# Kernel tuning notes

Hardware: AMD Instinct MI355X
Metric: run time of the kernel (lower is better)

Reference implementation:

```python
import jax, jax.numpy as jnp
import numpy as np

# Production-scale config (CIFAR-like images, PixelRNN Diagonal BiLSTM)
B, C, H, W = 32, 3, 32, 32
HC = 128   # hidden_channels
NC = 256   # num_classes


def _diag_indices(height, width):
    """Static index maps for anti-diagonal traversal of the skewed grid.

    skewed grid is (H, SW) with SW = W + H - 1. Diagonal d contains cells
    (row, col=d-row) for valid rows, processed in increasing-row order.
    Returns SW, row[D,S], col[D,S] (clipped), mask[D,S], rev[D,S] where
    rev[d, t] = len(d)-1-t maps forward step index <-> reversed step index.
    """
    SW = width + height - 1
    D = height + SW - 1
    d = np.arange(D)[:, None]
    s = np.arange(height)[None, :]
    r0 = np.maximum(0, d - (SW - 1))
    length = np.minimum(height - 1, d) - r0 + 1
    row = r0 + s
    col = d - row
    mask = s < length
    rev = np.clip(length - 1 - s, 0, height - 1)
    return SW, np.clip(row, 0, height - 1), np.clip(col, 0, SW - 1), mask, rev


def _lstm_scan(inp, mask, Wi, Wh, b):
    """Masked LSTM over all diagonals in parallel.

    inp: (B, D, S, in_dim) step-major per-diagonal inputs; mask: (D, S) bool.
    States are zero-initialized per diagonal (matching the torch module which
    resets states for every diagonal). Returns hidden outputs (B, D, S, hc).
    """
    Bb, Dd, S, _ = inp.shape
    hc = Wh.shape[1]

    def step(carry, xs):
        h, c = carry
        x_s, m = xs                       # (B, D, in_dim), (D,)
        gates = x_s @ Wi.T + b + h @ Wh.T  # (B, D, 4*hc)
        i, f, o, g = jnp.split(gates, 4, axis=-1)
        c_new = jax.nn.sigmoid(f) * c + jax.nn.sigmoid(i) * jnp.tanh(g)
        h_new = jax.nn.sigmoid(o) * jnp.tanh(c_new)
        m3 = m[None, :, None]
        return (jnp.where(m3, h_new, h), jnp.where(m3, c_new, c)), jnp.where(m3, h_new, 0.0)

    h0 = jnp.zeros((Bb, Dd, hc), inp.dtype)
    _, ys = jax.lax.scan(step, (h0, h0), (inp.transpose(2, 0, 1, 3), mask.T))
    return ys.transpose(1, 2, 0, 3)


def _forward(x, in_proj_w, in_proj_b, fwd_Wi, fwd_Wh, fwd_b,
             bwd_Wi, bwd_Wh, bwd_b, out_w, out_b):
    Bb, Cc, Hh, Ww = x.shape
    hc = in_proj_w.shape[0]
    nc = out_w.shape[0] // Cc
    SW, row, col, mask_np, rev_np = _diag_indices(Hh, Ww)
    rows = np.arange(Hh)
    cols_unskew = rows[:, None] + np.arange(Ww)[None, :]  # (H, W)

    # 1x1 input projection on normalized pixels
    xp = jnp.einsum('bchw,oc->bohw', x / 255.0, in_proj_w) + in_proj_b[None, :, None, None]

    # skew: row i shifted right by i
    skewed = jnp.zeros((Bb, hc, Hh, SW), xp.dtype).at[
        :, :, rows[:, None], cols_unskew].set(xp)

    mask = jnp.asarray(mask_np)
    # gather per-diagonal sequences: (B, D, S, hc)
    diag = jnp.where(mask[None, :, :, None],
                     skewed[:, :, row, col].transpose(0, 2, 3, 1), 0.0)

    # forward direction along each diagonal
    h_fwd = _lstm_scan(diag, mask, fwd_Wi, fwd_Wh, fwd_b)

    # backward direction: reverse steps within each diagonal, scan, un-reverse
    rev_idx = jnp.asarray(rev_np)[None, :, :, None]
    h_bwd_rev = _lstm_scan(jnp.take_along_axis(diag, rev_idx, axis=2),
                           mask, bwd_Wi, bwd_Wh, bwd_b)
    h_bwd = jnp.where(mask[None, :, :, None],
                      jnp.take_along_axis(h_bwd_rev, rev_idx, axis=2), 0.0)

    def to_grid(h):  # scatter (B, D, S, hc) back onto the skewed grid
        return jnp.zeros((Bb, hc, Hh, SW), h.dtype).at[
            :, :, row, col].add(h.transpose(0, 3, 1, 2))

    comb = jnp.concatenate([to_grid(h_fwd), to_grid(h_bwd)], axis=1)  # (B, 2hc, H, SW)

    # unskew: row i takes cols i:i+W
    un = comb[:, :, rows[:, None], cols_unskew]  # (B, 2hc, H, W)

    logits = jnp.einsum('bchw,oc->bohw', un, out_w) + out_b[None, :, None, None]
    return logits.reshape(Bb, Cc, nc, Hh, Ww)


def setup_inputs() -> dict:
    key = jax.random.key(0)
    ks = jax.random.split(key, 11)
    sc = 0.05
    return {
        'x': jax.random.uniform(ks[0], (B, C, H, W), jnp.float32) * 255.0,
        'in_proj_w': jax.random.normal(ks[1], (HC, C), jnp.float32) * sc,
        'in_proj_b': jax.random.normal(ks[2], (HC,), jnp.float32) * sc,
        'fwd_Wi': jax.random.normal(ks[3], (4 * HC, HC), jnp.float32) * sc,
        'fwd_Wh': jax.random.normal(ks[4], (4 * HC, HC), jnp.float32) * sc,
        'fwd_b': jax.random.normal(ks[5], (4 * HC,), jnp.float32) * sc,
        'bwd_Wi': jax.random.normal(ks[6], (4 * HC, HC), jnp.float32) * sc,
        'bwd_Wh': jax.random.normal(ks[7], (4 * HC, HC), jnp.float32) * sc,
        'bwd_b': jax.random.normal(ks[8], (4 * HC,), jnp.float32) * sc,
        'out_w': jax.random.normal(ks[9], (C * NC, 2 * HC), jnp.float32) * sc,
        'out_b': jax.random.normal(ks[10], (C * NC,), jnp.float32) * sc,
    }


def reference(x, in_proj_w, in_proj_b, fwd_Wi, fwd_Wh, fwd_b,
              bwd_Wi, bwd_Wh, bwd_b, out_w, out_b):
    return _forward(x, in_proj_w, in_proj_b, fwd_Wi, fwd_Wh, fwd_b,
                    bwd_Wi, bwd_Wh, bwd_b, out_w, out_b)
```

## Files before the change

kernel.cpp:

```cpp
#include <hip/hip_runtime.h>

#define Hh 32
#define Ww 32
#define SW 63
#define DD 94

typedef __attribute__((ext_vector_type(8))) short  s8v;
typedef __attribute__((ext_vector_type(4))) float  f32x4;


__device__ __forceinline__ float sigmoid_f(float v) {
    return 1.0f / (1.0f + __expf(-v));
}
__device__ __forceinline__ float tanh_f(float v) {
    float e = __expf(2.0f * v);
    return 1.0f - 2.0f / (e + 1.0f);
}
__device__ __forceinline__ unsigned short f2bf(float f) {
    unsigned int u = __builtin_bit_cast(unsigned int, f);
    unsigned int r = (u + 0x7fffu + ((u >> 16) & 1u)) >> 16;
    return (unsigned short)r;
}

__global__ void prep_wf(const float* __restrict__ fwi, const float* __restrict__ fwh,
                        const float* __restrict__ bwi, const float* __restrict__ bwh,
                        unsigned short* __restrict__ wif, unsigned short* __restrict__ whf) {
    int m = blockIdx.y;
    const float* src = (m == 0) ? fwi : (m == 1) ? fwh : (m == 2) ? bwi : bwh;
    unsigned short* dst = (m & 1) ? whf : wif;
    int dir = m >> 1;

    int t = blockIdx.x * 256 + threadIdx.x;
    int lane = t & 63;
    int kt   = (t >> 6) & 3;
    int nt   = (t >> 8) & 3;
    int wv   = (t >> 10) & 7;

    int gp = wv * 64 + nt * 16 + (lane & 15);
    int ch = gp >> 2, ty = gp & 3;
    int kbase = kt * 32 + (lane >> 4) * 8;
    const float* srow = src + (ty * 128 + ch) * 128 + kbase;

    s8v v;
    #pragma unroll
    for (int j = 0; j < 8; j++) v[j] = (short)f2bf(srow[j]);
    int off = dir * 65536 + ((wv * 4 + nt) * 4 + kt) * 512 + lane * 8;
    *reinterpret_cast<s8v*>(dst + off) = v;
}

__global__ void prep_b(const float* __restrict__ fwd_b, const float* __restrict__ bwd_b,
                       float* __restrict__ biasp) {
    int tid = threadIdx.x;
    int dir = tid >> 9;
    int gp  = tid & 511;
    int ch  = gp >> 2;
    int ty  = gp & 3;
    const float* src = dir ? bwd_b : fwd_b;
    biasp[dir * 512 + gp] = src[ty * 128 + ch];
}

__global__ void prep_ow(const float* __restrict__ ow, unsigned short* __restrict__ owb) {
    int i = blockIdx.x * 1024 + threadIdx.x;
    owb[i] = f2bf(ow[i]);
}

__global__ __launch_bounds__(512, 2) void lstm_mfma(
    const float* __restrict__ x,
    const float* __restrict__ ipw,
    const float* __restrict__ ipb,
    const unsigned short* __restrict__ whf,
    const unsigned short* __restrict__ wif,
    const float* __restrict__ biasp,
    unsigned short* __restrict__ comb)
{
    __shared__ unsigned short h_lds[2][32 * 128];
    __shared__ unsigned short xp_lds[2][32 * 128];
    __shared__ float ipw_s[384];
    __shared__ float ipb_s[128];

    const int tid  = threadIdx.x;
    const int wv   = tid >> 6;
    const int lane = tid & 63;
    const int g16  = lane >> 4;
    const int cl   = lane & 15;
    const int swz  = (cl & 7) << 3;

    const int d   = blockIdx.x >> 1;
    const int dir = blockIdx.x & 1;
    const int r0   = max(0, d - (SW - 1));
    const int rend = min(Hh - 1, d);
    const int len  = rend - r0 + 1;
    const float inv255 = 1.0f / 255.0f;

    s8v whB[4][4], wiB[4][4];
    {
        const unsigned short* whd = whf + dir * 65536;
        const unsigned short* wid = wif + dir * 65536;
        #pragma unroll
        for (int nt = 0; nt < 4; nt++)
            #pragma unroll
            for (int kt = 0; kt < 4; kt++) {
                int off = ((wv * 4 + nt) * 4 + kt) * 512 + lane * 8;
                whB[nt][kt] = *reinterpret_cast<const s8v*>(whd + off);
                wiB[nt][kt] = *reinterpret_cast<const s8v*>(wid + off);
            }
    }
    f32x4 bias4[4];
    #pragma unroll
    for (int nt = 0; nt < 4; nt++)
        bias4[nt] = *reinterpret_cast<const f32x4*>(biasp + dir * 512 + wv * 64 + nt * 16 + g16 * 4);

    if (tid < 384) ipw_s[tid] = ipw[tid];
    else if (tid < 512) ipb_s[tid - 384] = ipb[tid - 384];

    {
        unsigned int* hz = reinterpret_cast<unsigned int*>(&h_lds[0][0]);
        #pragma unroll
        for (int j = 0; j < 4; j++) hz[tid * 4 + j] = 0u;
    }
    __syncthreads();

    {
        int s0 = dir ? (len - 1) : 0;
        int row0 = r0 + s0;
        int w0 = d - 2 * row0;
        bool valid0 = ((unsigned)w0 < 32u);
        #pragma unroll
        for (int mt = 0; mt < 2; mt++) {
            int seq = mt * 16 + cl;
            float xv0 = 0, xv1 = 0, xv2 = 0;
            if (valid0) {
                const float* xb = x + seq * 3072 + row0 * 32 + w0;
                xv0 = xb[0]; xv1 = xb[1024]; xv2 = xb[2048];
            }
            #pragma unroll
            for (int nt = 0; nt < 4; nt++) {
                int ch = wv * 16 + nt * 4 + g16;
                float xpf = 0.0f;
                if (valid0)
                    xpf = ipb_s[ch] + inv255 * (xv0 * ipw_s[ch * 3] + xv1 * ipw_s[ch * 3 + 1] + xv2 * ipw_s[ch * 3 + 2]);
                xp_lds[0][(seq * 128 + ch) ^ swz] = f2bf(xpf);
            }
        }
    }
    __syncthreads();

    float cst[2][4];
    #pragma unroll
    for (int mt = 0; mt < 2; mt++)
        #pragma unroll
        for (int nt = 0; nt < 4; nt++) cst[mt][nt] = 0.0f;

    int cur = 0;
    for (int t = 0; t < len; t++) {
        int s   = dir ? (len - 1 - t) : t;
        int row = r0 + s;
        int w   = d - 2 * row;
        bool valid = ((unsigned)w < 32u);

        int s2 = dir ? (len - 2 - t) : (t + 1);
        bool have2 = (t + 1 < len);
        int row2 = r0 + s2;
        int w2 = d - 2 * row2;
        bool valid2 = have2 && ((unsigned)w2 < 32u);

        f32x4 acc[2][4];
        #pragma unroll
        for (int mt = 0; mt < 2; mt++)
            #pragma unroll
            for (int nt = 0; nt < 4; nt++) acc[mt][nt] = bias4[nt];

        #pragma unroll
        for (int kt = 0; kt < 4; kt++) {
            s8v hfr[2], xfr[2];
            #pragma unroll
            for (int mt = 0; mt < 2; mt++) {
                int idx = ((mt * 16 + cl) * 128 + kt * 32 + g16 * 8) ^ swz;
                hfr[mt] = *reinterpret_cast<const s8v*>(&h_lds[cur][idx]);
                xfr[mt] = *reinterpret_cast<const s8v*>(&xp_lds[cur][idx]);
            }
            #pragma unroll
            for (int mt = 0; mt < 2; mt++)
                #pragma unroll
                for (int nt = 0; nt < 4; nt++) {
                    acc[mt][nt] = __builtin_amdgcn_mfma_f32_16x16x32_bf16(whB[nt][kt], hfr[mt], acc[mt][nt], 0, 0, 0);
                    acc[mt][nt] = __builtin_amdgcn_mfma_f32_16x16x32_bf16(wiB[nt][kt], xfr[mt], acc[mt][nt], 0, 0, 0);
                }
        }

        int nxt = cur ^ 1;
        #pragma unroll
        for (int mt = 0; mt < 2; mt++) {
            int seq = mt * 16 + cl;
            float xv0 = 0, xv1 = 0, xv2 = 0;
            if (valid2) {
                const float* xb = x + seq * 3072 + row2 * 32 + w2;
                xv0 = xb[0]; xv1 = xb[1024]; xv2 = xb[2048];
            }
            #pragma unroll
            for (int nt = 0; nt < 4; nt++) {
                int ch = wv * 16 + nt * 4 + g16;
                float gi = acc[mt][nt][0];
                float gf = acc[mt][nt][1];
                float go = acc[mt][nt][2];
                float gg = acc[mt][nt][3];
                float c = sigmoid_f(gf) * cst[mt][nt] + sigmoid_f(gi) * tanh_f(gg);
                cst[mt][nt] = c;
                float hn = sigmoid_f(go) * tanh_f(c);
                unsigned short hq = f2bf(hn);

                int idx = (seq * 128 + ch) ^ swz;
                h_lds[nxt][idx] = hq;
                if (valid)
                    comb[((seq * 32 + row) * 32 + w) * 256 + dir * 128 + ch] = hq;
                if (have2) {
                    float xpf = 0.0f;
                    if (valid2)
                        xpf = ipb_s[ch] + inv255 * (xv0 * ipw_s[ch * 3] + xv1 * ipw_s[ch * 3 + 1] + xv2 * ipw_s[ch * 3 + 2]);
                    xp_lds[nxt][idx] = f2bf(xpf);
                }
            }
        }
        __syncthreads();
        cur = nxt;
    }
}

__global__ __launch_bounds__(256) void outproj_mfma(
    const unsigned short* __restrict__ comb,
    const unsigned short* __restrict__ owb,
    const float* __restrict__ ob,
    float* __restrict__ out)
{
    const int tid  = threadIdx.x;
    const int wave = tid >> 6;
    const int wo   = wave >> 1;
    const int wc   = wave & 1;
    const int lane = tid & 63;
    const int g16  = lane >> 4;
    const int cl   = lane & 15;

    const int o_base = blockIdx.y * 128 + wo * 64;
    const int c_base = blockIdx.x * 128 + wc * 64;

    f32x4 acc[4][4];
    #pragma unroll
    for (int of = 0; of < 4; of++)
        #pragma unroll
        for (int cf = 0; cf < 4; cf++) {
            f32x4 z = {0.f, 0.f, 0.f, 0.f};
            acc[of][cf] = z;
        }

    for (int kt = 0; kt < 8; kt++) {
        int kb = kt * 32 + g16 * 8;
        s8v a[4], b[4];
        #pragma unroll
        for (int of = 0; of < 4; of++)
            a[of] = *reinterpret_cast<const s8v*>(owb + (o_base + of * 16 + cl) * 256 + kb);
        #pragma unroll
        for (int cf = 0; cf < 4; cf++)
            b[cf] = *reinterpret_cast<const s8v*>(comb + (c_base + cf * 16 + cl) * 256 + kb);
        #pragma unroll
        for (int of = 0; of < 4; of++)
            #pragma unroll
            for (int cf = 0; cf < 4; cf++)
                acc[of][cf] = __builtin_amdgcn_mfma_f32_16x16x32_bf16(a[of], b[cf], acc[of][cf], 0, 0, 0);
    }

    #pragma unroll
    for (int of = 0; of < 4; of++) {
        f32x4 obv = *reinterpret_cast<const f32x4*>(ob + o_base + of * 16 + g16 * 4);
        #pragma unroll
        for (int cf = 0; cf < 4; cf++) {
            int cell = c_base + cf * 16 + cl;
            int bi = cell >> 10;
            int rw = cell & 1023;
            #pragma unroll
            for (int r = 0; r < 4; r++) {
                int o = o_base + of * 16 + g16 * 4 + r;
                out[(bi * 768 + o) * 1024 + rw] = acc[of][cf][r] + obv[r];
            }
        }
    }
}

extern "C" void kernel_launch(void* const* d_in, const int* in_sizes, int n_in,
                              void* d_out, int out_size, void* d_ws, size_t ws_size,
                              hipStream_t stream) {
    const float* x      = (const float*)d_in[0];
    const float* ipw    = (const float*)d_in[1];
    const float* ipb    = (const float*)d_in[2];
    const float* fwd_Wi = (const float*)d_in[3];
    const float* fwd_Wh = (const float*)d_in[4];
    const float* fwd_b  = (const float*)d_in[5];
    const float* bwd_Wi = (const float*)d_in[6];
    const float* bwd_Wh = (const float*)d_in[7];
    const float* bwd_b  = (const float*)d_in[8];
    const float* out_w  = (const float*)d_in[9];
    const float* out_b  = (const float*)d_in[10];

    char* ws = (char*)d_ws;
    unsigned short* whf   = (unsigned short*)(ws);
    unsigned short* wif   = (unsigned short*)(ws + (256 << 10));
    float*          biasp = (float*)(ws + (512 << 10));
    unsigned short* owb   = (unsigned short*)(ws + (768 << 10));
    unsigned short* comb  = (unsigned short*)(ws + (2 << 20));
    float*          out   = (float*)d_out;

    hipLaunchKernelGGL(prep_wf, dim3(64, 4), dim3(256), 0, stream,
                       fwd_Wi, fwd_Wh, bwd_Wi, bwd_Wh, wif, whf);
    hipLaunchKernelGGL(prep_b, dim3(1), dim3(1024), 0, stream,
                       fwd_b, bwd_b, biasp);
    hipLaunchKernelGGL(prep_ow, dim3(192), dim3(1024), 0, stream,
                       out_w, owb);

    hipLaunchKernelGGL(lstm_mfma, dim3(DD * 2), dim3(512), 0, stream,
                       x, ipw, ipb, whf, wif, biasp, comb);

    hipLaunchKernelGGL(outproj_mfma, dim3(256, 6), dim3(256), 0, stream,
                       comb, owb, out_b, out);
}
```

Measured before the change: 320.6 us.

## Fold input projection into Wi, precompute padding-cell LSTM states, split batch across blocks

Folds the 3-channel input projection into the LSTM input weights so the input gate contribution becomes a rank-3 affine per step, which removes the Wi MFMAs and the xp LDS buffer. Padding cells, whose input is zero, are handled by a precomputed table of h/c states after j leading padding steps, so each diagonal block runs only its valid rows. The batch is split into two 16-sequence blocks and each wave now covers 8 gate tiles, which raises the grid size. The output projection epilogue is staged through LDS so global stores are coalesced. This adds a serial single-block prep kernel and keeps the input path in fp32, so rounding differs slightly from the old bf16 path.

```diff
diff --git a/kernel.cpp b/kernel.cpp
--- a/kernel.cpp
+++ b/kernel.cpp
@@ -1,7 +1,5 @@
 #include <hip/hip_runtime.h>
 
-#define Hh 32
-#define Ww 32
 #define SW 63
 #define DD 94
 
@@ -22,41 +20,87 @@
     return (unsigned short)r;
 }
 
-__global__ void prep_wf(const float* __restrict__ fwi, const float* __restrict__ fwh,
-                        const float* __restrict__ bwi, const float* __restrict__ bwh,
-                        unsigned short* __restrict__ wif, unsigned short* __restrict__ whf) {
-    int m = blockIdx.y;
-    const float* src = (m == 0) ? fwi : (m == 1) ? fwh : (m == 2) ? bwi : bwh;
-    unsigned short* dst = (m & 1) ? whf : wif;
-    int dir = m >> 1;
-
+__global__ void prep_whf(const float* __restrict__ fwh, const float* __restrict__ bwh,
+                         unsigned short* __restrict__ whf) {
+    int dir = blockIdx.y;
+    const float* src = dir ? bwh : fwh;
     int t = blockIdx.x * 256 + threadIdx.x;
     int lane = t & 63;
     int kt   = (t >> 6) & 3;
-    int nt   = (t >> 8) & 3;
-    int wv   = (t >> 10) & 7;
-
-    int gp = wv * 64 + nt * 16 + (lane & 15);
-    int ch = gp >> 2, ty = gp & 3;
-    int kbase = kt * 32 + (lane >> 4) * 8;
-    const float* srow = src + (ty * 128 + ch) * 128 + kbase;
-
+    int nt   = (t >> 8) & 7;
+    int wv   = (t >> 11) & 3;
+    int gp  = wv * 128 + nt * 16 + (lane & 15);
+    int row = (gp & 3) * 128 + (gp >> 2);
+    int kb  = kt * 32 + (lane >> 4) * 8;
+    const float* sr = src + row * 128 + kb;
     s8v v;
     #pragma unroll
-    for (int j = 0; j < 8; j++) v[j] = (short)f2bf(srow[j]);
-    int off = dir * 65536 + ((wv * 4 + nt) * 4 + kt) * 512 + lane * 8;
-    *reinterpret_cast<s8v*>(dst + off) = v;
-}
-
-__global__ void prep_b(const float* __restrict__ fwd_b, const float* __restrict__ bwd_b,
-                       float* __restrict__ biasp) {
+    for (int j = 0; j < 8; j++) v[j] = (short)f2bf(sr[j]);
+    *reinterpret_cast<s8v*>(whf + dir * 65536 + ((wv * 8 + nt) * 4 + kt) * 512 + lane * 8) = v;
+}
+
+__global__ void prep_m1(const float* __restrict__ fwi, const float* __restrict__ bwi,
+                        const float* __restrict__ fb,  const float* __restrict__ bb,
+                        const float* __restrict__ ipw, const float* __restrict__ ipb,
+                        float* __restrict__ m1g) {
+    int t = blockIdx.x * 256 + threadIdx.x;
+    int dir = t >> 9;
+    int gp  = t & 511;
+    const float* Wi = dir ? bwi : fwi;
+    const float* bs = dir ? bb  : fb;
+    int row = (gp & 3) * 128 + (gp >> 2);
+    const float* wr = Wi + row * 128;
+    float m0 = 0, m1 = 0, m2 = 0, b2 = bs[row];
+    for (int k = 0; k < 128; k++) {
+        float wv = wr[k];
+        m0 += wv * ipw[k * 3 + 0];
+        m1 += wv * ipw[k * 3 + 1];
+        m2 += wv * ipw[k * 3 + 2];
+        b2 += wv * ipb[k];
+    }
+    const float inv255 = 1.0f / 255.0f;
+    float* d = m1g + (dir * 512 + gp) * 4;
+    d[0] = m0 * inv255; d[1] = m1 * inv255; d[2] = m2 * inv255; d[3] = b2;
+}
+
+__global__ void prep_padtab(const float* __restrict__ fwh, const float* __restrict__ bwh,
+                            const float* __restrict__ fb,  const float* __restrict__ bb,
+                            float* __restrict__ padtab) {
+    __shared__ float h_s[2][128], c_s[2][128], g_s[2][512];
     int tid = threadIdx.x;
     int dir = tid >> 9;
-    int gp  = tid & 511;
-    int ch  = gp >> 2;
-    int ty  = gp & 3;
-    const float* src = dir ? bwd_b : fwd_b;
-    biasp[dir * 512 + gp] = src[ty * 128 + ch];
+    int go  = tid & 511;
+    const float* Wh = dir ? bwh : fwh;
+    const float* bs = dir ? bb  : fb;
+    float bias = bs[go];
+    if (go < 128) {
+        h_s[dir][go] = 0.0f; c_s[dir][go] = 0.0f;
+        padtab[(dir * 17) * 256 + go] = 0.0f;
+        padtab[(dir * 17) * 256 + 128 + go] = 0.0f;
+    }
+    __syncthreads();
+    const float* wr = Wh + go * 128;
+    for (int j = 1; j <= 16; j++) {
+        float acc = bias;
+        for (int k = 0; k < 128; k += 4) {
+            float4 w4 = *(const float4*)(wr + k);
+            acc += w4.x * h_s[dir][k] + w4.y * h_s[dir][k + 1]
+                 + w4.z * h_s[dir][k + 2] + w4.w * h_s[dir][k + 3];
+        }
+        g_s[dir][go] = acc;
+        __syncthreads();
+        if (go < 128) {
+            int ch = go;
+            float gi = g_s[dir][ch], gf = g_s[dir][128 + ch];
+            float gO = g_s[dir][256 + ch], gg = g_s[dir][384 + ch];
+            float c = sigmoid_f(gf) * c_s[dir][ch] + sigmoid_f(gi) * tanh_f(gg);
+            float h = sigmoid_f(gO) * tanh_f(c);
+            h_s[dir][ch] = h; c_s[dir][ch] = c;
+            padtab[(dir * 17 + j) * 256 + ch] = h;
+            padtab[(dir * 17 + j) * 256 + 128 + ch] = c;
+        }
+        __syncthreads();
+    }
 }
 
 __global__ void prep_ow(const float* __restrict__ ow, unsigned short* __restrict__ owb) {
@@ -64,19 +108,15 @@
     owb[i] = f2bf(ow[i]);
 }
 
-__global__ __launch_bounds__(512, 2) void lstm_mfma(
+__global__ __launch_bounds__(256, 2) void lstm_diag(
     const float* __restrict__ x,
-    const float* __restrict__ ipw,
-    const float* __restrict__ ipb,
     const unsigned short* __restrict__ whf,
-    const unsigned short* __restrict__ wif,
-    const float* __restrict__ biasp,
+    const float* __restrict__ m1g,
+    const float* __restrict__ padtab,
     unsigned short* __restrict__ comb)
 {
-    __shared__ unsigned short h_lds[2][32 * 128];
-    __shared__ unsigned short xp_lds[2][32 * 128];
-    __shared__ float ipw_s[384];
-    __shared__ float ipb_s[128];
+    __shared__ unsigned short h_lds[2][16 * 128];
+    __shared__ float m1_s[512 * 4];
 
     const int tid  = threadIdx.x;
     const int wv   = tid >> 6;
@@ -85,141 +125,103 @@
     const int cl   = lane & 15;
     const int swz  = (cl & 7) << 3;
 
-    const int d   = blockIdx.x >> 1;
-    const int dir = blockIdx.x & 1;
-    const int r0   = max(0, d - (SW - 1));
-    const int rend = min(Hh - 1, d);
-    const int len  = rend - r0 + 1;
-    const float inv255 = 1.0f / 255.0f;
-
-    s8v whB[4][4], wiB[4][4];
+    const int bidx = blockIdx.x;
+    const int d    = bidx >> 2;
+    const int dir  = (bidx >> 1) & 1;
+    const int bh   = bidx & 1;
+
+    const int r0   = max(0, d - 62);
+    const int rend = min(31, d);
+    int a = d - 31;
+    const int rlo = max(r0, (a > 0) ? ((a + 1) >> 1) : 0);
+    const int rhi = min(rend, d >> 1);
+    const int nv  = rhi - rlo + 1;
+    const int jlead = dir ? (rend - rhi) : (rlo - r0);
+
     {
-        const unsigned short* whd = whf + dir * 65536;
-        const unsigned short* wid = wif + dir * 65536;
-        #pragma unroll
-        for (int nt = 0; nt < 4; nt++)
-            #pragma unroll
-            for (int kt = 0; kt < 4; kt++) {
-                int off = ((wv * 4 + nt) * 4 + kt) * 512 + lane * 8;
-                whB[nt][kt] = *reinterpret_cast<const s8v*>(whd + off);
-                wiB[nt][kt] = *reinterpret_cast<const s8v*>(wid + off);
+        const f32x4* src = reinterpret_cast<const f32x4*>(m1g + dir * 2048);
+        f32x4* dst = reinterpret_cast<f32x4*>(m1_s);
+        dst[tid * 2]     = src[tid * 2];
+        dst[tid * 2 + 1] = src[tid * 2 + 1];
+    }
+    {
+        const float* ph = padtab + (dir * 17 + jlead) * 256;
+        #pragma unroll
+        for (int i = 0; i < 8; i++) {
+            int l = tid * 8 + i;
+            int seq = l >> 7, ch = l & 127;
+            h_lds[0][l ^ ((seq & 7) << 3)] = f2bf(ph[ch]);
+        }
+    }
+    s8v whB[8][4];
+    {
+        const unsigned short* wp = whf + dir * 65536;
+        #pragma unroll
+        for (int nt = 0; nt < 8; nt++)
+            #pragma unroll
+            for (int kt = 0; kt < 4; kt++)
+                whB[nt][kt] = *reinterpret_cast<const s8v*>(
+                    wp + ((wv * 8 + nt) * 4 + kt) * 512 + lane * 8);
+    }
+    float cst[8];
+    {
+        const float* pc = padtab + (dir * 17 + jlead) * 256 + 128;
+        #pragma unroll
+        for (int nt = 0; nt < 8; nt++) cst[nt] = pc[wv * 32 + nt * 4 + g16];
+    }
+    __syncthreads();
+
+    const int b = bh * 16 + cl;
+    const float* xb = x + b * 3072;
+
+    int rowp = dir ? rhi : rlo;
+    int wp_  = d - 2 * rowp;
+    float xv0 = xb[rowp * 32 + wp_];
+    float xv1 = xb[1024 + rowp * 32 + wp_];
+    float xv2 = xb[2048 + rowp * 32 + wp_];
+
+    int cur = 0;
+    for (int t = 0; t < nv; t++) {
+        int rowc = dir ? (rhi - t) : (rlo + t);
+        int wc_  = d - 2 * rowc;
+
+        f32x4 acc[8];
+        #pragma unroll
+        for (int nt = 0; nt < 8; nt++) {
+            #pragma unroll
+            for (int r = 0; r < 4; r++) {
+                f32x4 m = *reinterpret_cast<const f32x4*>(
+                    &m1_s[(wv * 128 + nt * 16 + g16 * 4 + r) * 4]);
+                acc[nt][r] = m[3] + xv0 * m[0] + xv1 * m[1] + xv2 * m[2];
             }
-    }
-    f32x4 bias4[4];
-    #pragma unroll
-    for (int nt = 0; nt < 4; nt++)
-        bias4[nt] = *reinterpret_cast<const f32x4*>(biasp + dir * 512 + wv * 64 + nt * 16 + g16 * 4);
-
-    if (tid < 384) ipw_s[tid] = ipw[tid];
-    else if (tid < 512) ipb_s[tid - 384] = ipb[tid - 384];
-
-    {
-        unsigned int* hz = reinterpret_cast<unsigned int*>(&h_lds[0][0]);
-        #pragma unroll
-        for (int j = 0; j < 4; j++) hz[tid * 4 + j] = 0u;
-    }
-    __syncthreads();
-
-    {
-        int s0 = dir ? (len - 1) : 0;
-        int row0 = r0 + s0;
-        int w0 = d - 2 * row0;
-        bool valid0 = ((unsigned)w0 < 32u);
-        #pragma unroll
-        for (int mt = 0; mt < 2; mt++) {
-            int seq = mt * 16 + cl;
-            float xv0 = 0, xv1 = 0, xv2 = 0;
-            if (valid0) {
-                const float* xb = x + seq * 3072 + row0 * 32 + w0;
-                xv0 = xb[0]; xv1 = xb[1024]; xv2 = xb[2048];
-            }
-            #pragma unroll
-            for (int nt = 0; nt < 4; nt++) {
-                int ch = wv * 16 + nt * 4 + g16;
-                float xpf = 0.0f;
-                if (valid0)
-                    xpf = ipb_s[ch] + inv255 * (xv0 * ipw_s[ch * 3] + xv1 * ipw_s[ch * 3 + 1] + xv2 * ipw_s[ch * 3 + 2]);
-                xp_lds[0][(seq * 128 + ch) ^ swz] = f2bf(xpf);
-            }
-        }
-    }
-    __syncthreads();
-
-    float cst[2][4];
-    #pragma unroll
-    for (int mt = 0; mt < 2; mt++)
-        #pragma unroll
-        for (int nt = 0; nt < 4; nt++) cst[mt][nt] = 0.0f;
-
-    int cur = 0;
-    for (int t = 0; t < len; t++) {
-        int s   = dir ? (len - 1 - t) : t;
-        int row = r0 + s;
-        int w   = d - 2 * row;
-        bool valid = ((unsigned)w < 32u);
-
-        int s2 = dir ? (len - 2 - t) : (t + 1);
-        bool have2 = (t + 1 < len);
-        int row2 = r0 + s2;
-        int w2 = d - 2 * row2;
-        bool valid2 = have2 && ((unsigned)w2 < 32u);
-
-        f32x4 acc[2][4];
-        #pragma unroll
-        for (int mt = 0; mt < 2; mt++)
-            #pragma unroll
-            for (int nt = 0; nt < 4; nt++) acc[mt][nt] = bias4[nt];
-
+        }
         #pragma unroll
         for (int kt = 0; kt < 4; kt++) {
-            s8v hfr[2], xfr[2];
-            #pragma unroll
-            for (int mt = 0; mt < 2; mt++) {
-                int idx = ((mt * 16 + cl) * 128 + kt * 32 + g16 * 8) ^ swz;
-                hfr[mt] = *reinterpret_cast<const s8v*>(&h_lds[cur][idx]);
-                xfr[mt] = *reinterpret_cast<const s8v*>(&xp_lds[cur][idx]);
-            }
-            #pragma unroll
-            for (int mt = 0; mt < 2; mt++)
-                #pragma unroll
-                for (int nt = 0; nt < 4; nt++) {
-                    acc[mt][nt] = __builtin_amdgcn_mfma_f32_16x16x32_bf16(whB[nt][kt], hfr[mt], acc[mt][nt], 0, 0, 0);
-                    acc[mt][nt] = __builtin_amdgcn_mfma_f32_16x16x32_bf16(wiB[nt][kt], xfr[mt], acc[mt][nt], 0, 0, 0);
-                }
-        }
-
+            int idx = (cl * 128 + kt * 32 + g16 * 8) ^ swz;
+            s8v hf = *reinterpret_cast<const s8v*>(&h_lds[cur][idx]);
+            #pragma unroll
+            for (int nt = 0; nt < 8; nt++)
+                acc[nt] = __builtin_amdgcn_mfma_f32_16x16x32_bf16(whB[nt][kt], hf, acc[nt], 0, 0, 0);
+        }
+        if (t + 1 < nv) {
+            int rn = dir ? (rhi - t - 1) : (rlo + t + 1);
+            int wn = d - 2 * rn;
+            xv0 = xb[rn * 32 + wn];
+            xv1 = xb[1024 + rn * 32 + wn];
+            xv2 = xb[2048 + rn * 32 + wn];
+        }
         int nxt = cur ^ 1;
-        #pragma unroll
-        for (int mt = 0; mt < 2; mt++) {
-            int seq = mt * 16 + cl;
-            float xv0 = 0, xv1 = 0, xv2 = 0;
-            if (valid2) {
-                const float* xb = x + seq * 3072 + row2 * 32 + w2;
-                xv0 = xb[0]; xv1 = xb[1024]; xv2 = xb[2048];
-            }
-            #pragma unroll
-            for (int nt = 0; nt < 4; nt++) {
-                int ch = wv * 16 + nt * 4 + g16;
-                float gi = acc[mt][nt][0];
-                float gf = acc[mt][nt][1];
-                float go = acc[mt][nt][2];
-                float gg = acc[mt][nt][3];
-                float c = sigmoid_f(gf) * cst[mt][nt] + sigmoid_f(gi) * tanh_f(gg);
-                cst[mt][nt] = c;
-                float hn = sigmoid_f(go) * tanh_f(c);
-                unsigned short hq = f2bf(hn);
-
-                int idx = (seq * 128 + ch) ^ swz;
-                h_lds[nxt][idx] = hq;
-                if (valid)
-                    comb[((seq * 32 + row) * 32 + w) * 256 + dir * 128 + ch] = hq;
-                if (have2) {
-                    float xpf = 0.0f;
-                    if (valid2)
-                        xpf = ipb_s[ch] + inv255 * (xv0 * ipw_s[ch * 3] + xv1 * ipw_s[ch * 3 + 1] + xv2 * ipw_s[ch * 3 + 2]);
-                    xp_lds[nxt][idx] = f2bf(xpf);
-                }
-            }
+        unsigned int cbase = ((unsigned)(b * 32 + rowc) * 32 + wc_) * 256 + dir * 128;
+        #pragma unroll
+        for (int nt = 0; nt < 8; nt++) {
+            int ch = wv * 32 + nt * 4 + g16;
+            float gi = acc[nt][0], gf = acc[nt][1], gO = acc[nt][2], gg = acc[nt][3];
+            float c = sigmoid_f(gf) * cst[nt] + sigmoid_f(gi) * tanh_f(gg);
+            cst[nt] = c;
+            float hn = sigmoid_f(gO) * tanh_f(c);
+            unsigned short hq = f2bf(hn);
+            h_lds[nxt][(cl * 128 + ch) ^ swz] = hq;
+            comb[cbase + ch] = hq;
         }
         __syncthreads();
         cur = nxt;
@@ -232,6 +234,8 @@
     const float* __restrict__ ob,
     float* __restrict__ out)
 {
+    __shared__ float ep[32 * 132];
+
     const int tid  = threadIdx.x;
     const int wave = tid >> 6;
     const int wo   = wave >> 1;
@@ -254,33 +258,41 @@
 
     for (int kt = 0; kt < 8; kt++) {
         int kb = kt * 32 + g16 * 8;
-        s8v a[4], b[4];
+        s8v av[4], bv[4];
         #pragma unroll
         for (int of = 0; of < 4; of++)
-            a[of] = *reinterpret_cast<const s8v*>(owb + (o_base + of * 16 + cl) * 256 + kb);
+            av[of] = *reinterpret_cast<const s8v*>(owb + (o_base + of * 16 + cl) * 256 + kb);
         #pragma unroll
         for (int cf = 0; cf < 4; cf++)
-            b[cf] = *reinterpret_cast<const s8v*>(comb + (c_base + cf * 16 + cl) * 256 + kb);
+            bv[cf] = *reinterpret_cast<const s8v*>(comb + (c_base + cf * 16 + cl) * 256 + kb);
         #pragma unroll
         for (int of = 0; of < 4; of++)
             #pragma unroll
             for (int cf = 0; cf < 4; cf++)
-                acc[of][cf] = __builtin_amdgcn_mfma_f32_16x16x32_bf16(a[of], b[cf], acc[of][cf], 0, 0, 0);
-    }
-
+                acc[of][cf] = __builtin_amdgcn_mfma_f32_16x16x32_bf16(av[of], bv[cf], acc[of][cf], 0, 0, 0);
+    }
+
+    const int bi  = (blockIdx.x * 128) >> 10;
+    const int rwb = (blockIdx.x * 128) & 1023;
     #pragma unroll
     for (int of = 0; of < 4; of++) {
-        f32x4 obv = *reinterpret_cast<const f32x4*>(ob + o_base + of * 16 + g16 * 4);
-        #pragma unroll
-        for (int cf = 0; cf < 4; cf++) {
-            int cell = c_base + cf * 16 + cl;
-            int bi = cell >> 10;
-            int rw = cell & 1023;
-            #pragma unroll
-            for (int r = 0; r < 4; r++) {
-                int o = o_base + of * 16 + g16 * 4 + r;
-                out[(bi * 768 + o) * 1024 + rw] = acc[of][cf][r] + obv[r];
-            }
+        __syncthreads();
+        #pragma unroll
+        for (int cf = 0; cf < 4; cf++)
+            #pragma unroll
+            for (int r = 0; r < 4; r++)
+                ep[(wo * 16 + g16 * 4 + r) * 132 + wc * 64 + cf * 16 + cl] = acc[of][cf][r];
+        __syncthreads();
+        int o_loc = tid >> 3;
+        int cs    = (tid & 7) * 16;
+        int o     = blockIdx.y * 128 + (o_loc >> 4) * 64 + of * 16 + (o_loc & 15);
+        float bo  = ob[o];
+        float* op = out + (bi * 768 + o) * 1024 + rwb + cs;
+        #pragma unroll
+        for (int i = 0; i < 4; i++) {
+            f32x4 v = *reinterpret_cast<const f32x4*>(&ep[o_loc * 132 + cs + i * 4]);
+            v[0] += bo; v[1] += bo; v[2] += bo; v[3] += bo;
+            *reinterpret_cast<f32x4*>(op + i * 4) = v;
         }
     }
 }
@@ -301,22 +313,24 @@
     const float* out_b  = (const float*)d_in[10];
 
     char* ws = (char*)d_ws;
-    unsigned short* whf   = (unsigned short*)(ws);
-    unsigned short* wif   = (unsigned short*)(ws + (256 << 10));
-    float*          biasp = (float*)(ws + (512 << 10));
-    unsigned short* owb   = (unsigned short*)(ws + (768 << 10));
-    unsigned short* comb  = (unsigned short*)(ws + (2 << 20));
-    float*          out   = (float*)d_out;
-
-    hipLaunchKernelGGL(prep_wf, dim3(64, 4), dim3(256), 0, stream,
-                       fwd_Wi, fwd_Wh, bwd_Wi, bwd_Wh, wif, whf);
-    hipLaunchKernelGGL(prep_b, dim3(1), dim3(1024), 0, stream,
-                       fwd_b, bwd_b, biasp);
+    unsigned short* whf    = (unsigned short*)(ws);
+    float*          m1g    = (float*)(ws + (256 << 10));
+    float*          padtab = (float*)(ws + (288 << 10));
+    unsigned short* owb    = (unsigned short*)(ws + (512 << 10));
+    unsigned short* comb   = (unsigned short*)(ws + (1 << 20));
+    float*          out    = (float*)d_out;
+
+    hipLaunchKernelGGL(prep_whf, dim3(32, 2), dim3(256), 0, stream,
+                       fwd_Wh, bwd_Wh, whf);
+    hipLaunchKernelGGL(prep_m1, dim3(4), dim3(256), 0, stream,
+                       fwd_Wi, bwd_Wi, fwd_b, bwd_b, ipw, ipb, m1g);
+    hipLaunchKernelGGL(prep_padtab, dim3(1), dim3(1024), 0, stream,
+                       fwd_Wh, bwd_Wh, fwd_b, bwd_b, padtab);
     hipLaunchKernelGGL(prep_ow, dim3(192), dim3(1024), 0, stream,
                        out_w, owb);
 
-    hipLaunchKernelGGL(lstm_mfma, dim3(DD * 2), dim3(512), 0, stream,
-                       x, ipw, ipb, whf, wif, biasp, comb);
+    hipLaunchKernelGGL(lstm_diag, dim3(DD * 4), dim3(256), 0, stream,
+                       x, whf, m1g, padtab, comb);
 
     hipLaunchKernelGGL(outproj_mfma, dim3(256, 6), dim3(256), 0, stream,
                        comb, owb, out_b, out);
```

After: 328.0 us. +2.3%, slower.
